# Performance work log

Measured on AMD Instinct MI355X. Metric: run time of the kernel, lower is better.

Reference implementation:

```python
import jax, jax.numpy as jnp
import numpy as np

N_GRID = 262144   # grid vertices (all local, empty halo)
N_MESH = 40962    # icosahedral mesh level-6 vertices
N_EDGES = 524288  # mesh2grid bipartite edges
H = 128           # cfg.model.hidden_dim
LN_EPS = 1e-5


def layer_norm(x, g, b):
    m = jnp.mean(x, axis=-1, keepdims=True)
    v = jnp.var(x, axis=-1, keepdims=True)
    return (x - m) * jax.lax.rsqrt(v + LN_EPS) * g + b


def setup_inputs() -> dict:
    key = jax.random.key(0)
    ks = jax.random.split(key, 12)
    def w(k, shape, fan_in):
        return jax.random.normal(k, shape, jnp.float32) * (fan_in ** -0.5)
    return {
        "mesh2grid_edge_features": jax.random.normal(ks[0], (N_EDGES, H), jnp.float32),
        "grid_node_features": jax.random.normal(ks[1], (N_GRID, H), jnp.float32),
        "mesh_node_features": jax.random.normal(ks[2], (N_MESH, H), jnp.float32),
        # edge MLP: Linear(3H->H) -> SiLU -> Linear(H->H) -> LayerNorm, residual
        "edge_W1": w(ks[3], (3 * H, H), 3 * H), "edge_b1": jnp.zeros((H,), jnp.float32),
        "edge_W2": w(ks[4], (H, H), H), "edge_b2": jnp.zeros((H,), jnp.float32),
        "edge_ln_g": jnp.ones((H,), jnp.float32), "edge_ln_b": jnp.zeros((H,), jnp.float32),
        # node MLP: Linear(2H->H) -> SiLU -> Linear(H->H) -> LayerNorm
        "node_W1": w(ks[5], (2 * H, H), 2 * H), "node_b1": jnp.zeros((H,), jnp.float32),
        "node_W2": w(ks[6], (H, H), H), "node_b2": jnp.zeros((H,), jnp.float32),
        "node_ln_g": jnp.ones((H,), jnp.float32), "node_ln_b": jnp.zeros((H,), jnp.float32),
        "src_indices": jax.random.randint(ks[7], (N_EDGES,), 0, N_MESH, jnp.int32),
        "dst_indices": jax.random.randint(ks[8], (N_EDGES,), 0, N_GRID, jnp.int32),
    }


def reference(mesh2grid_edge_features, grid_node_features, mesh_node_features,
              edge_W1, edge_b1, edge_W2, edge_b2, edge_ln_g, edge_ln_b,
              node_W1, node_b1, node_W2, node_b2, node_ln_g, node_ln_b,
              src_indices, dst_indices):
    # --- edge block: gather src (mesh) / dst (grid), MLP, LN, residual ---
    src = mesh_node_features[src_indices]        # [E, H]  (augmented mesh == mesh, empty halo)
    dst = grid_node_features[dst_indices]        # [E, H]
    xe = jnp.concatenate([src, dst, mesh2grid_edge_features], axis=-1)  # [E, 3H]
    he = (jax.nn.silu(xe @ edge_W1 + edge_b1)) @ edge_W2 + edge_b2
    e_feats = mesh2grid_edge_features + layer_norm(he, edge_ln_g, edge_ln_b)  # [E, H]
    # --- node block: scatter-sum edges to grid nodes, MLP, LN ---
    agg = jax.ops.segment_sum(e_feats, dst_indices, num_segments=N_GRID)  # [N_grid, H]
    xn = jnp.concatenate([grid_node_features, agg], axis=-1)              # [N_grid, 2H]
    hn = (jax.nn.silu(xn @ node_W1 + node_b1)) @ node_W2 + node_b2
    n_feats = layer_norm(hn, node_ln_g, node_ln_b)
    return grid_node_features + n_feats
```

## Files before the change

kernel.cpp:

```cpp
#include <hip/hip_runtime.h>
#include <stdint.h>

#define HDIM 128
#define NGRID 262144
#define NMESH 40962
#define NEDGE 524288

typedef __attribute__((ext_vector_type(8))) short short8;
typedef __attribute__((ext_vector_type(4))) float f32x4;

__device__ __forceinline__ unsigned short f2bf(float f) {
  union { float f; uint32_t u; } v; v.f = f;
  uint32_t u = v.u;
  u += 0x7fffu + ((u >> 16) & 1u);
  return (unsigned short)(u >> 16);
}
__device__ __forceinline__ float bf2f(unsigned short h) {
  union { uint32_t u; float f; } v; v.u = ((uint32_t)h) << 16;
  return v.f;
}

__global__ void pack_weights(const float* __restrict__ eW1, const float* __restrict__ eW2,
                             const float* __restrict__ nW1, const float* __restrict__ nW2,
                             unsigned short* __restrict__ ws)
{
  int i = blockIdx.x * 256 + threadIdx.x;
  unsigned short* eW1T = ws;
  unsigned short* eW2T = ws + 49152;
  unsigned short* nW1T = ws + 65536;
  unsigned short* nW2T = ws + 98304;
  if (i < 49152) {
    int c = i / 384, k = i % 384;
    eW1T[i] = f2bf(eW1[(size_t)k * 128 + c]);
  } else if (i < 65536) {
    int j = i - 49152; int c = j / 128, k = j % 128;
    eW2T[j] = f2bf(eW2[(size_t)k * 128 + c]);
  } else if (i < 98304) {
    int j = i - 65536; int c = j / 256, k = j % 256;
    nW1T[j] = f2bf(nW1[(size_t)k * 128 + c]);
  } else if (i < 114688) {
    int j = i - 98304; int c = j / 128, k = j % 128;
    nW2T[j] = f2bf(nW2[(size_t)k * 128 + c]);
  }
}

__global__ __launch_bounds__(256)
void edge_kernel(const float* __restrict__ ef, const float* __restrict__ gridf,
                 const float* __restrict__ mesh,
                 const unsigned short* __restrict__ W1T, const unsigned short* __restrict__ W2T,
                 const float* __restrict__ b1, const float* __restrict__ b2,
                 const float* __restrict__ lng, const float* __restrict__ lnb,
                 const int* __restrict__ src, const int* __restrict__ dst,
                 float* __restrict__ agg)
{
  __shared__ __align__(16) unsigned short xe[64][392];
  __shared__ __align__(16) unsigned short h1s[64][136];
  __shared__ __align__(16) unsigned short wt[128][40];
  __shared__ int sidx[64];
  __shared__ int didx[64];

  const int tid = threadIdx.x;
  const int wave = tid >> 6;
  const int lane = tid & 63;
  const int l16 = lane & 15;
  const int g4 = lane >> 4;
  const int e0 = blockIdx.x * 64;

  if (tid < 64) sidx[tid] = src[e0 + tid];
  else if (tid < 128) didx[tid - 64] = dst[e0 + tid - 64];
  __syncthreads();

  {
    const int l32 = lane & 31;
    const int sub = lane >> 5;
    for (int i = 0; i < 24; ++i) {
      int rc = ((wave * 24 + i) << 1) | sub;
      int part = rc >> 6;
      int e = rc & 63;
      const float* base;
      if (part == 0)      base = mesh  + (size_t)sidx[e] * HDIM;
      else if (part == 1) base = gridf + (size_t)didx[e] * HDIM;
      else                base = ef    + (size_t)(e0 + e) * HDIM;
      float4 v = reinterpret_cast<const float4*>(base)[l32];
      ushort4 o;
      o.x = f2bf(v.x); o.y = f2bf(v.y); o.z = f2bf(v.z); o.w = f2bf(v.w);
      *reinterpret_cast<ushort4*>(&xe[e][part * 128 + l32 * 4]) = o;
    }
  }
  __syncthreads();

  const int arow = wave * 16 + l16;
  const int stg_r = tid >> 1, stg_h = tid & 1;

  f32x4 acc[8];
  #pragma unroll
  for (int c = 0; c < 8; ++c) acc[c] = (f32x4){0.f, 0.f, 0.f, 0.f};

  for (int ks = 0; ks < 12; ++ks) {
    {
      const unsigned short* gp = W1T + (size_t)stg_r * 384 + ks * 32 + stg_h * 16;
      uint4 a0 = *reinterpret_cast<const uint4*>(gp);
      uint4 a1 = *reinterpret_cast<const uint4*>(gp + 8);
      unsigned short* dp = &wt[stg_r][stg_h * 16];
      *reinterpret_cast<uint4*>(dp) = a0;
      *reinterpret_cast<uint4*>(dp + 8) = a1;
    }
    __syncthreads();
    short8 a = *reinterpret_cast<const short8*>(&xe[arow][ks * 32 + g4 * 8]);
    #pragma unroll
    for (int c = 0; c < 8; ++c) {
      short8 b = *reinterpret_cast<const short8*>(&wt[c * 16 + l16][g4 * 8]);
      acc[c] = __builtin_amdgcn_mfma_f32_16x16x32_bf16(a, b, acc[c], 0, 0, 0);
    }
    __syncthreads();
  }

  #pragma unroll
  for (int c = 0; c < 8; ++c) {
    int col = c * 16 + l16;
    float bb = b1[col];
    #pragma unroll
    for (int r = 0; r < 4; ++r) {
      float x = acc[c][r] + bb;
      float s = x / (1.f + __expf(-x));
      h1s[wave * 16 + g4 * 4 + r][col] = f2bf(s);
    }
  }
  __syncthreads();

  f32x4 acc2[8];
  #pragma unroll
  for (int c = 0; c < 8; ++c) acc2[c] = (f32x4){0.f, 0.f, 0.f, 0.f};

  for (int ks = 0; ks < 4; ++ks) {
    {
      const unsigned short* gp = W2T + (size_t)stg_r * 128 + ks * 32 + stg_h * 16;
      uint4 a0 = *reinterpret_cast<const uint4*>(gp);
      uint4 a1 = *reinterpret_cast<const uint4*>(gp + 8);
      unsigned short* dp = &wt[stg_r][stg_h * 16];
      *reinterpret_cast<uint4*>(dp) = a0;
      *reinterpret_cast<uint4*>(dp + 8) = a1;
    }
    __syncthreads();
    short8 a = *reinterpret_cast<const short8*>(&h1s[arow][ks * 32 + g4 * 8]);
    #pragma unroll
    for (int c = 0; c < 8; ++c) {
      short8 b = *reinterpret_cast<const short8*>(&wt[c * 16 + l16][g4 * 8]);
      acc2[c] = __builtin_amdgcn_mfma_f32_16x16x32_bf16(a, b, acc2[c], 0, 0, 0);
    }
    __syncthreads();
  }

  float vs[4] = {0.f, 0.f, 0.f, 0.f};
  float vq[4] = {0.f, 0.f, 0.f, 0.f};
  #pragma unroll
  for (int c = 0; c < 8; ++c) {
    float bb = b2[c * 16 + l16];
    #pragma unroll
    for (int r = 0; r < 4; ++r) {
      float x = acc2[c][r] + bb;
      acc2[c][r] = x;
      vs[r] += x;
      vq[r] += x * x;
    }
  }
  #pragma unroll
  for (int m = 1; m < 16; m <<= 1) {
    #pragma unroll
    for (int r = 0; r < 4; ++r) {
      vs[r] += __shfl_xor(vs[r], m);
      vq[r] += __shfl_xor(vq[r], m);
    }
  }
  float mean[4], rstd[4];
  #pragma unroll
  for (int r = 0; r < 4; ++r) {
    mean[r] = vs[r] * (1.f / 128.f);
    float var = vq[r] * (1.f / 128.f) - mean[r] * mean[r];
    rstd[r] = rsqrtf(var + 1e-5f);
  }
  #pragma unroll
  for (int c = 0; c < 8; ++c) {
    int col = c * 16 + l16;
    float gg = lng[col], bb = lnb[col];
    #pragma unroll
    for (int r = 0; r < 4; ++r) {
      int row = wave * 16 + g4 * 4 + r;
      float y = (acc2[c][r] - mean[r]) * rstd[r] * gg + bb;
      float e = bf2f(xe[row][256 + col]) + y;
      atomicAdd(&agg[(size_t)didx[row] * HDIM + col], e);
    }
  }
}

__global__ __launch_bounds__(256)
void node_kernel(const float* __restrict__ gridf,
                 const unsigned short* __restrict__ W1T, const unsigned short* __restrict__ W2T,
                 const float* __restrict__ b1, const float* __restrict__ b2,
                 const float* __restrict__ lng, const float* __restrict__ lnb,
                 float* __restrict__ out)
{
  __shared__ __align__(16) unsigned short xn[64][264];
  __shared__ __align__(16) unsigned short h1s[64][136];
  __shared__ __align__(16) unsigned short wt[128][40];

  const int tid = threadIdx.x;
  const int wave = tid >> 6;
  const int lane = tid & 63;
  const int l16 = lane & 15;
  const int g4 = lane >> 4;
  const int n0 = blockIdx.x * 64;

  {
    const int l32 = lane & 31;
    const int sub = lane >> 5;
    for (int i = 0; i < 16; ++i) {
      int rc = ((wave * 16 + i) << 1) | sub;
      int part = rc >> 6;
      int e = rc & 63;
      const float* base = (part == 0) ? gridf + (size_t)(n0 + e) * HDIM
                                      : out   + (size_t)(n0 + e) * HDIM;
      float4 v = reinterpret_cast<const float4*>(base)[l32];
      ushort4 o;
      o.x = f2bf(v.x); o.y = f2bf(v.y); o.z = f2bf(v.z); o.w = f2bf(v.w);
      *reinterpret_cast<ushort4*>(&xn[e][part * 128 + l32 * 4]) = o;
    }
  }
  __syncthreads();

  const int arow = wave * 16 + l16;
  const int stg_r = tid >> 1, stg_h = tid & 1;

  f32x4 acc[8];
  #pragma unroll
  for (int c = 0; c < 8; ++c) acc[c] = (f32x4){0.f, 0.f, 0.f, 0.f};

  for (int ks = 0; ks < 8; ++ks) {
    {
      const unsigned short* gp = W1T + (size_t)stg_r * 256 + ks * 32 + stg_h * 16;
      uint4 a0 = *reinterpret_cast<const uint4*>(gp);
      uint4 a1 = *reinterpret_cast<const uint4*>(gp + 8);
      unsigned short* dp = &wt[stg_r][stg_h * 16];
      *reinterpret_cast<uint4*>(dp) = a0;
      *reinterpret_cast<uint4*>(dp + 8) = a1;
    }
    __syncthreads();
    short8 a = *reinterpret_cast<const short8*>(&xn[arow][ks * 32 + g4 * 8]);
    #pragma unroll
    for (int c = 0; c < 8; ++c) {
      short8 b = *reinterpret_cast<const short8*>(&wt[c * 16 + l16][g4 * 8]);
      acc[c] = __builtin_amdgcn_mfma_f32_16x16x32_bf16(a, b, acc[c], 0, 0, 0);
    }
    __syncthreads();
  }

  #pragma unroll
  for (int c = 0; c < 8; ++c) {
    int col = c * 16 + l16;
    float bb = b1[col];
    #pragma unroll
    for (int r = 0; r < 4; ++r) {
      float x = acc[c][r] + bb;
      float s = x / (1.f + __expf(-x));
      h1s[wave * 16 + g4 * 4 + r][col] = f2bf(s);
    }
  }
  __syncthreads();

  f32x4 acc2[8];
  #pragma unroll
  for (int c = 0; c < 8; ++c) acc2[c] = (f32x4){0.f, 0.f, 0.f, 0.f};

  for (int ks = 0; ks < 4; ++ks) {
    {
      const unsigned short* gp = W2T + (size_t)stg_r * 128 + ks * 32 + stg_h * 16;
      uint4 a0 = *reinterpret_cast<const uint4*>(gp);
      uint4 a1 = *reinterpret_cast<const uint4*>(gp + 8);
      unsigned short* dp = &wt[stg_r][stg_h * 16];
      *reinterpret_cast<uint4*>(dp) = a0;
      *reinterpret_cast<uint4*>(dp + 8) = a1;
    }
    __syncthreads();
    short8 a = *reinterpret_cast<const short8*>(&h1s[arow][ks * 32 + g4 * 8]);
    #pragma unroll
    for (int c = 0; c < 8; ++c) {
      short8 b = *reinterpret_cast<const short8*>(&wt[c * 16 + l16][g4 * 8]);
      acc2[c] = __builtin_amdgcn_mfma_f32_16x16x32_bf16(a, b, acc2[c], 0, 0, 0);
    }
    __syncthreads();
  }

  float vs[4] = {0.f, 0.f, 0.f, 0.f};
  float vq[4] = {0.f, 0.f, 0.f, 0.f};
  #pragma unroll
  for (int c = 0; c < 8; ++c) {
    float bb = b2[c * 16 + l16];
    #pragma unroll
    for (int r = 0; r < 4; ++r) {
      float x = acc2[c][r] + bb;
      acc2[c][r] = x;
      vs[r] += x;
      vq[r] += x * x;
    }
  }
  #pragma unroll
  for (int m = 1; m < 16; m <<= 1) {
    #pragma unroll
    for (int r = 0; r < 4; ++r) {
      vs[r] += __shfl_xor(vs[r], m);
      vq[r] += __shfl_xor(vq[r], m);
    }
  }
  float mean[4], rstd[4];
  #pragma unroll
  for (int r = 0; r < 4; ++r) {
    mean[r] = vs[r] * (1.f / 128.f);
    float var = vq[r] * (1.f / 128.f) - mean[r] * mean[r];
    rstd[r] = rsqrtf(var + 1e-5f);
  }
  #pragma unroll
  for (int c = 0; c < 8; ++c) {
    int col = c * 16 + l16;
    float gg = lng[col], bb = lnb[col];
    #pragma unroll
    for (int r = 0; r < 4; ++r) {
      int row = wave * 16 + g4 * 4 + r;
      size_t idx = (size_t)(n0 + row) * HDIM + col;
      float y = (acc2[c][r] - mean[r]) * rstd[r] * gg + bb;
      out[idx] = gridf[idx] + y;
    }
  }
}

extern "C" void kernel_launch(void* const* d_in, const int* in_sizes, int n_in,
                              void* d_out, int out_size, void* d_ws, size_t ws_size,
                              hipStream_t stream)
{
  (void)in_sizes; (void)n_in; (void)out_size; (void)ws_size;
  const float* ef   = (const float*)d_in[0];
  const float* grid = (const float*)d_in[1];
  const float* mesh = (const float*)d_in[2];
  const float* eW1  = (const float*)d_in[3];
  const float* eb1  = (const float*)d_in[4];
  const float* eW2  = (const float*)d_in[5];
  const float* eb2  = (const float*)d_in[6];
  const float* elng = (const float*)d_in[7];
  const float* elnb = (const float*)d_in[8];
  const float* nW1  = (const float*)d_in[9];
  const float* nb1  = (const float*)d_in[10];
  const float* nW2  = (const float*)d_in[11];
  const float* nb2  = (const float*)d_in[12];
  const float* nlng = (const float*)d_in[13];
  const float* nlnb = (const float*)d_in[14];
  const int* src    = (const int*)d_in[15];
  const int* dst    = (const int*)d_in[16];
  float* out = (float*)d_out;
  unsigned short* ws = (unsigned short*)d_ws;

  hipMemsetAsync(out, 0, (size_t)NGRID * HDIM * sizeof(float), stream);
  pack_weights<<<448, 256, 0, stream>>>(eW1, eW2, nW1, nW2, ws);
  edge_kernel<<<NEDGE / 64, 256, 0, stream>>>(ef, grid, mesh,
      ws, ws + 49152, eb1, eb2, elng, elnb, src, dst, out);
  node_kernel<<<NGRID / 64, 256, 0, stream>>>(grid,
      ws + 65536, ws + 98304, nb1, nb2, nlng, nlnb, out);
}
```

Measured before the change: 794.5 us.

## Load MFMA operands straight from global memory, dropping shared-memory staging and barriers

Both edge and node kernels now read activation rows and bf16 weight fragments directly from global memory into MFMA operand registers, instead of staging them through shared memory with a barrier around every k-step. Shared memory is kept only for the hidden activation tile, and those writes are packed in pairs via lane shuffles. The edge residual is re-read as fp32 from global, atomics become unsafeAtomicAdd, and launch bounds request 4 blocks per SM. The aim is to cut LDS traffic and sync stalls and raise occupancy. The cost is more global/L2 traffic for weights that are no longer reused across waves, and uncoalesced 32-byte per-lane gathers.

```diff
diff --git a/kernel.cpp b/kernel.cpp
--- a/kernel.cpp
+++ b/kernel.cpp
@@ -18,6 +18,14 @@
 __device__ __forceinline__ float bf2f(unsigned short h) {
   union { uint32_t u; float f; } v; v.u = ((uint32_t)h) << 16;
   return v.f;
+}
+__device__ __forceinline__ short8 cvt8(float4 a, float4 b) {
+  short8 r;
+  r[0] = (short)f2bf(a.x); r[1] = (short)f2bf(a.y);
+  r[2] = (short)f2bf(a.z); r[3] = (short)f2bf(a.w);
+  r[4] = (short)f2bf(b.x); r[5] = (short)f2bf(b.y);
+  r[6] = (short)f2bf(b.z); r[7] = (short)f2bf(b.w);
+  return r;
 }
 
 __global__ void pack_weights(const float* __restrict__ eW1, const float* __restrict__ eW2,
@@ -44,7 +52,7 @@
   }
 }
 
-__global__ __launch_bounds__(256)
+__global__ __launch_bounds__(256, 4)
 void edge_kernel(const float* __restrict__ ef, const float* __restrict__ gridf,
                  const float* __restrict__ mesh,
                  const unsigned short* __restrict__ W1T, const unsigned short* __restrict__ W2T,
@@ -53,77 +61,60 @@
                  const int* __restrict__ src, const int* __restrict__ dst,
                  float* __restrict__ agg)
 {
-  __shared__ __align__(16) unsigned short xe[64][392];
   __shared__ __align__(16) unsigned short h1s[64][136];
-  __shared__ __align__(16) unsigned short wt[128][40];
-  __shared__ int sidx[64];
-  __shared__ int didx[64];
-
-  const int tid = threadIdx.x;
+
+  const int tid  = threadIdx.x;
   const int wave = tid >> 6;
   const int lane = tid & 63;
-  const int l16 = lane & 15;
-  const int g4 = lane >> 4;
-  const int e0 = blockIdx.x * 64;
-
-  if (tid < 64) sidx[tid] = src[e0 + tid];
-  else if (tid < 128) didx[tid - 64] = dst[e0 + tid - 64];
-  __syncthreads();
-
-  {
-    const int l32 = lane & 31;
-    const int sub = lane >> 5;
-    for (int i = 0; i < 24; ++i) {
-      int rc = ((wave * 24 + i) << 1) | sub;
-      int part = rc >> 6;
-      int e = rc & 63;
-      const float* base;
-      if (part == 0)      base = mesh  + (size_t)sidx[e] * HDIM;
-      else if (part == 1) base = gridf + (size_t)didx[e] * HDIM;
-      else                base = ef    + (size_t)(e0 + e) * HDIM;
-      float4 v = reinterpret_cast<const float4*>(base)[l32];
-      ushort4 o;
-      o.x = f2bf(v.x); o.y = f2bf(v.y); o.z = f2bf(v.z); o.w = f2bf(v.w);
-      *reinterpret_cast<ushort4*>(&xe[e][part * 128 + l32 * 4]) = o;
-    }
-  }
-  __syncthreads();
-
+  const int l16  = lane & 15;
+  const int g4   = lane >> 4;
+  const int e0   = blockIdx.x * 64;
   const int arow = wave * 16 + l16;
-  const int stg_r = tid >> 1, stg_h = tid & 1;
+
+  const int myS = src[e0 + arow];
+  const int myD = dst[e0 + arow];
+  const float* rowS = mesh  + (size_t)myS * HDIM;
+  const float* rowD = gridf + (size_t)myD * HDIM;
+  const float* rowE = ef    + (size_t)(e0 + arow) * HDIM;
 
   f32x4 acc[8];
   #pragma unroll
   for (int c = 0; c < 8; ++c) acc[c] = (f32x4){0.f, 0.f, 0.f, 0.f};
 
-  for (int ks = 0; ks < 12; ++ks) {
-    {
-      const unsigned short* gp = W1T + (size_t)stg_r * 384 + ks * 32 + stg_h * 16;
-      uint4 a0 = *reinterpret_cast<const uint4*>(gp);
-      uint4 a1 = *reinterpret_cast<const uint4*>(gp + 8);
-      unsigned short* dp = &wt[stg_r][stg_h * 16];
-      *reinterpret_cast<uint4*>(dp) = a0;
-      *reinterpret_cast<uint4*>(dp + 8) = a1;
-    }
-    __syncthreads();
-    short8 a = *reinterpret_cast<const short8*>(&xe[arow][ks * 32 + g4 * 8]);
-    #pragma unroll
-    for (int c = 0; c < 8; ++c) {
-      short8 b = *reinterpret_cast<const short8*>(&wt[c * 16 + l16][g4 * 8]);
-      acc[c] = __builtin_amdgcn_mfma_f32_16x16x32_bf16(a, b, acc[c], 0, 0, 0);
-    }
-    __syncthreads();
-  }
-
-  #pragma unroll
-  for (int c = 0; c < 8; ++c) {
-    int col = c * 16 + l16;
+  const unsigned short* wl1 = W1T + (size_t)l16 * 384 + g4 * 8;
+
+  #pragma unroll
+  for (int part = 0; part < 3; ++part) {
+    const float* base = (part == 0) ? rowS : (part == 1) ? rowD : rowE;
+    #pragma unroll
+    for (int kk = 0; kk < 4; ++kk) {
+      const int ks = part * 4 + kk;
+      const float* ap = base + kk * 32 + g4 * 8;
+      float4 f0 = *reinterpret_cast<const float4*>(ap);
+      float4 f1 = *reinterpret_cast<const float4*>(ap + 4);
+      short8 a = cvt8(f0, f1);
+      #pragma unroll
+      for (int c = 0; c < 8; ++c) {
+        short8 b = *reinterpret_cast<const short8*>(wl1 + (size_t)c * 16 * 384 + ks * 32);
+        acc[c] = __builtin_amdgcn_mfma_f32_16x16x32_bf16(a, b, acc[c], 0, 0, 0);
+      }
+    }
+  }
+
+  #pragma unroll
+  for (int c = 0; c < 8; ++c) {
+    const int col = c * 16 + l16;
     float bb = b1[col];
     #pragma unroll
     for (int r = 0; r < 4; ++r) {
       float x = acc[c][r] + bb;
       float s = x / (1.f + __expf(-x));
-      h1s[wave * 16 + g4 * 4 + r][col] = f2bf(s);
+      unsigned int h = f2bf(s);
+      unsigned int other = __shfl_xor((int)h, 1);
+      unsigned int packed = (l16 & 1) ? ((h << 16) | other) : ((other << 16) | h);
+      if ((l16 & 1) == (r & 1)) {
+        *reinterpret_cast<unsigned int*>(&h1s[wave * 16 + g4 * 4 + r][c * 16 + (l16 & ~1)]) = packed;
+      }
     }
   }
   __syncthreads();
@@ -132,23 +123,15 @@
   #pragma unroll
   for (int c = 0; c < 8; ++c) acc2[c] = (f32x4){0.f, 0.f, 0.f, 0.f};
 
+  const unsigned short* wl2 = W2T + (size_t)l16 * 128 + g4 * 8;
+  #pragma unroll
   for (int ks = 0; ks < 4; ++ks) {
-    {
-      const unsigned short* gp = W2T + (size_t)stg_r * 128 + ks * 32 + stg_h * 16;
-      uint4 a0 = *reinterpret_cast<const uint4*>(gp);
-      uint4 a1 = *reinterpret_cast<const uint4*>(gp + 8);
-      unsigned short* dp = &wt[stg_r][stg_h * 16];
-      *reinterpret_cast<uint4*>(dp) = a0;
-      *reinterpret_cast<uint4*>(dp + 8) = a1;
-    }
-    __syncthreads();
     short8 a = *reinterpret_cast<const short8*>(&h1s[arow][ks * 32 + g4 * 8]);
     #pragma unroll
     for (int c = 0; c < 8; ++c) {
-      short8 b = *reinterpret_cast<const short8*>(&wt[c * 16 + l16][g4 * 8]);
+      short8 b = *reinterpret_cast<const short8*>(wl2 + (size_t)c * 16 * 128 + ks * 32);
       acc2[c] = __builtin_amdgcn_mfma_f32_16x16x32_bf16(a, b, acc2[c], 0, 0, 0);
     }
-    __syncthreads();
   }
 
   float vs[4] = {0.f, 0.f, 0.f, 0.f};
@@ -179,90 +162,82 @@
     float var = vq[r] * (1.f / 128.f) - mean[r] * mean[r];
     rstd[r] = rsqrtf(var + 1e-5f);
   }
-  #pragma unroll
-  for (int c = 0; c < 8; ++c) {
-    int col = c * 16 + l16;
+  int drow[4];
+  #pragma unroll
+  for (int r = 0; r < 4; ++r) drow[r] = dst[e0 + wave * 16 + g4 * 4 + r];
+
+  #pragma unroll
+  for (int c = 0; c < 8; ++c) {
+    const int col = c * 16 + l16;
     float gg = lng[col], bb = lnb[col];
     #pragma unroll
     for (int r = 0; r < 4; ++r) {
-      int row = wave * 16 + g4 * 4 + r;
+      const int row = wave * 16 + g4 * 4 + r;
       float y = (acc2[c][r] - mean[r]) * rstd[r] * gg + bb;
-      float e = bf2f(xe[row][256 + col]) + y;
-      atomicAdd(&agg[(size_t)didx[row] * HDIM + col], e);
-    }
-  }
-}
-
-__global__ __launch_bounds__(256)
+      float e = ef[(size_t)(e0 + row) * HDIM + col] + y;
+      unsafeAtomicAdd(&agg[(size_t)drow[r] * HDIM + col], e);
+    }
+  }
+}
+
+__global__ __launch_bounds__(256, 4)
 void node_kernel(const float* __restrict__ gridf,
                  const unsigned short* __restrict__ W1T, const unsigned short* __restrict__ W2T,
                  const float* __restrict__ b1, const float* __restrict__ b2,
                  const float* __restrict__ lng, const float* __restrict__ lnb,
                  float* __restrict__ out)
 {
-  __shared__ __align__(16) unsigned short xn[64][264];
   __shared__ __align__(16) unsigned short h1s[64][136];
-  __shared__ __align__(16) unsigned short wt[128][40];
-
-  const int tid = threadIdx.x;
+
+  const int tid  = threadIdx.x;
   const int wave = tid >> 6;
   const int lane = tid & 63;
-  const int l16 = lane & 15;
-  const int g4 = lane >> 4;
-  const int n0 = blockIdx.x * 64;
-
-  {
-    const int l32 = lane & 31;
-    const int sub = lane >> 5;
-    for (int i = 0; i < 16; ++i) {
-      int rc = ((wave * 16 + i) << 1) | sub;
-      int part = rc >> 6;
-      int e = rc & 63;
-      const float* base = (part == 0) ? gridf + (size_t)(n0 + e) * HDIM
-                                      : out   + (size_t)(n0 + e) * HDIM;
-      float4 v = reinterpret_cast<const float4*>(base)[l32];
-      ushort4 o;
-      o.x = f2bf(v.x); o.y = f2bf(v.y); o.z = f2bf(v.z); o.w = f2bf(v.w);
-      *reinterpret_cast<ushort4*>(&xn[e][part * 128 + l32 * 4]) = o;
-    }
-  }
-  __syncthreads();
-
+  const int l16  = lane & 15;
+  const int g4   = lane >> 4;
+  const int n0   = blockIdx.x * 64;
   const int arow = wave * 16 + l16;
-  const int stg_r = tid >> 1, stg_h = tid & 1;
+
+  const float* rowG = gridf + (size_t)(n0 + arow) * HDIM;
+  const float* rowA = out   + (size_t)(n0 + arow) * HDIM;
 
   f32x4 acc[8];
   #pragma unroll
   for (int c = 0; c < 8; ++c) acc[c] = (f32x4){0.f, 0.f, 0.f, 0.f};
 
-  for (int ks = 0; ks < 8; ++ks) {
-    {
-      const unsigned short* gp = W1T + (size_t)stg_r * 256 + ks * 32 + stg_h * 16;
-      uint4 a0 = *reinterpret_cast<const uint4*>(gp);
-      uint4 a1 = *reinterpret_cast<const uint4*>(gp + 8);
-      unsigned short* dp = &wt[stg_r][stg_h * 16];
-      *reinterpret_cast<uint4*>(dp) = a0;
-      *reinterpret_cast<uint4*>(dp + 8) = a1;
-    }
-    __syncthreads();
-    short8 a = *reinterpret_cast<const short8*>(&xn[arow][ks * 32 + g4 * 8]);
-    #pragma unroll
-    for (int c = 0; c < 8; ++c) {
-      short8 b = *reinterpret_cast<const short8*>(&wt[c * 16 + l16][g4 * 8]);
-      acc[c] = __builtin_amdgcn_mfma_f32_16x16x32_bf16(a, b, acc[c], 0, 0, 0);
-    }
-    __syncthreads();
-  }
-
-  #pragma unroll
-  for (int c = 0; c < 8; ++c) {
-    int col = c * 16 + l16;
+  const unsigned short* wl1 = W1T + (size_t)l16 * 256 + g4 * 8;
+
+  #pragma unroll
+  for (int part = 0; part < 2; ++part) {
+    const float* base = (part == 0) ? rowG : rowA;
+    #pragma unroll
+    for (int kk = 0; kk < 4; ++kk) {
+      const int ks = part * 4 + kk;
+      const float* ap = base + kk * 32 + g4 * 8;
+      float4 f0 = *reinterpret_cast<const float4*>(ap);
+      float4 f1 = *reinterpret_cast<const float4*>(ap + 4);
+      short8 a = cvt8(f0, f1);
+      #pragma unroll
+      for (int c = 0; c < 8; ++c) {
+        short8 b = *reinterpret_cast<const short8*>(wl1 + (size_t)c * 16 * 256 + ks * 32);
+        acc[c] = __builtin_amdgcn_mfma_f32_16x16x32_bf16(a, b, acc[c], 0, 0, 0);
+      }
+    }
+  }
+
+  #pragma unroll
+  for (int c = 0; c < 8; ++c) {
+    const int col = c * 16 + l16;
     float bb = b1[col];
     #pragma unroll
     for (int r = 0; r < 4; ++r) {
       float x = acc[c][r] + bb;
       float s = x / (1.f + __expf(-x));
-      h1s[wave * 16 + g4 * 4 + r][col] = f2bf(s);
+      unsigned int h = f2bf(s);
+      unsigned int other = __shfl_xor((int)h, 1);
+      unsigned int packed = (l16 & 1) ? ((h << 16) | other) : ((other << 16) | h);
+      if ((l16 & 1) == (r & 1)) {
+        *reinterpret_cast<unsigned int*>(&h1s[wave * 16 + g4 * 4 + r][c * 16 + (l16 & ~1)]) = packed;
+      }
     }
   }
   __syncthreads();
@@ -271,23 +246,15 @@
   #pragma unroll
   for (int c = 0; c < 8; ++c) acc2[c] = (f32x4){0.f, 0.f, 0.f, 0.f};
 
+  const unsigned short* wl2 = W2T + (size_t)l16 * 128 + g4 * 8;
+  #pragma unroll
   for (int ks = 0; ks < 4; ++ks) {
-    {
-      const unsigned short* gp = W2T + (size_t)stg_r * 128 + ks * 32 + stg_h * 16;
-      uint4 a0 = *reinterpret_cast<const uint4*>(gp);
-      uint4 a1 = *reinterpret_cast<const uint4*>(gp + 8);
-      unsigned short* dp = &wt[stg_r][stg_h * 16];
-      *reinterpret_cast<uint4*>(dp) = a0;
-      *reinterpret_cast<uint4*>(dp + 8) = a1;
-    }
-    __syncthreads();
     short8 a = *reinterpret_cast<const short8*>(&h1s[arow][ks * 32 + g4 * 8]);
     #pragma unroll
     for (int c = 0; c < 8; ++c) {
-      short8 b = *reinterpret_cast<const short8*>(&wt[c * 16 + l16][g4 * 8]);
+      short8 b = *reinterpret_cast<const short8*>(wl2 + (size_t)c * 16 * 128 + ks * 32);
       acc2[c] = __builtin_amdgcn_mfma_f32_16x16x32_bf16(a, b, acc2[c], 0, 0, 0);
     }
-    __syncthreads();
   }
 
   float vs[4] = {0.f, 0.f, 0.f, 0.f};
@@ -320,11 +287,11 @@
   }
   #pragma unroll
   for (int c = 0; c < 8; ++c) {
-    int col = c * 16 + l16;
+    const int col = c * 16 + l16;
     float gg = lng[col], bb = lnb[col];
     #pragma unroll
     for (int r = 0; r < 4; ++r) {
-      int row = wave * 16 + g4 * 4 + r;
+      const int row = wave * 16 + g4 * 4 + r;
       size_t idx = (size_t)(n0 + row) * HDIM + col;
       float y = (acc2[c][r] - mean[r]) * rstd[r] * gg + bb;
       out[idx] = gridf[idx] + y;
```

Result: slower. 957.4 us (+20.5%).
